# Kernel tuning notes

Hardware: AMD Instinct MI355X
Metric: run time of the kernel (lower is better)

Reference implementation:

```python
import jax, jax.numpy as jnp
import numpy as np

N_LOOPS, B, L, V = 4, 4, 256, 50257

def setup_inputs() -> dict:
    key = jax.random.key(0)
    k1, k2, k3, k4 = jax.random.split(key, 4)
    logits = jax.random.normal(k1, (N_LOOPS, B, L, V), dtype=jnp.float32)
    input_ids = jax.random.randint(k2, (B, L), 0, V)
    ans_starts = jax.random.randint(k3, (B,), 1, L)
    # draw chain targets from tokens that actually appear in input_ids so the
    # restricted-vocab validity check (tgt in unique(input_ids[b])) passes
    pos = jax.random.randint(k4, (B, N_LOOPS), 0, L)
    chain_targets = jnp.take_along_axis(input_ids, pos, axis=1)  # [B, N_LOOPS]
    return {"logits": logits, "input_ids": input_ids,
            "ans_starts": ans_starts, "chain_targets": chain_targets}

def reference(logits, input_ids, ans_starts, chain_targets):
    # logits:        [n_loops, B, L, V]  per-loop lm_head outputs
    # input_ids:     [B, L] int
    # ans_starts:    [B] int (answer position; logits read at as_-1)
    # chain_targets: [B, n_loops] int target token ids per loop
    n_loops, Bb, Ll, Vv = logits.shape
    # restricted-vocab mask: 0 where token appears in the prompt, -inf elsewhere
    # (replaces the per-sample torch.unique + scatter loop)
    valid_tok = jnp.zeros((Bb, Vv), dtype=bool).at[
        jnp.arange(Bb)[:, None], input_ids].set(True)          # [B, V]
    mask = jnp.where(valid_tok, 0.0, -jnp.inf)                  # [B, V]

    as_idx = jnp.clip(ans_starts - 1, 0, Ll - 1)                # [B]
    # gather logits at the answer position for every loop: [n_loops, B, V]
    la = logits[:, jnp.arange(Bb), as_idx, :]
    masked = la + mask[None]                                    # [n_loops, B, V]

    tgt = chain_targets.T                                       # [n_loops, B]
    pos_ok = (ans_starts >= 1) & (ans_starts < Ll)              # [B]
    tgt_ok = valid_tok[jnp.arange(Bb)[None, :], tgt]            # [n_loops, B]
    valid = pos_ok[None, :] & tgt_ok                            # [n_loops, B]

    pred = jnp.argmax(masked, axis=-1)                          # [n_loops, B]
    safe_tgt = jnp.where(valid, tgt, pred)  # keep CE finite for invalid rows
    logp = jax.nn.log_softmax(masked, axis=-1)
    ce = -jnp.take_along_axis(logp, safe_tgt[..., None], axis=-1)[..., 0]
    acc = (pred == tgt).astype(jnp.float32)

    vf = valid.astype(jnp.float32)
    cnt = vf.sum(axis=1)                                        # [n_loops]
    loop_loss = (ce * vf).sum(axis=1) / jnp.maximum(cnt, 1.0)
    loop_acc = (acc * vf).sum(axis=1) / jnp.maximum(cnt, 1.0)
    has = (cnt > 0).astype(jnp.float32)
    n_valid_loops = jnp.maximum(has.sum(), 1.0)
    avg_loss = (loop_loss * has).sum() / n_valid_loops
    avg_acc = (loop_acc * has).sum() / n_valid_loops
    final_loop_acc = loop_acc[-1]
    return avg_loss, avg_acc, final_loop_acc
```

## Files before the change

kernel.cpp:

```cpp
#include <hip/hip_runtime.h>
#include <hip/hip_bf16.h>
#include <math.h>


#define NL 4
#define BB 4
#define LL 256
#define VV 50257
#define VWORDS ((VV + 31) / 32)
#define TPB 1024

__global__ __launch_bounds__(TPB) void rowstat_kernel(
    const float* __restrict__ logits,
    const int* __restrict__ input_ids,
    const int* __restrict__ ans_starts,
    const int* __restrict__ chain_targets,
    float* __restrict__ ws)
{
    const int nb = blockIdx.x;
    const int n = nb / BB;
    const int b = nb % BB;
    const int tid = threadIdx.x;

    __shared__ unsigned bitmap[VWORDS];
    __shared__ float sm[TPB];
    __shared__ float ss[TPB];
    __shared__ int   si[TPB];

    for (int i = tid; i < VWORDS; i += TPB) bitmap[i] = 0u;
    __syncthreads();
    for (int i = tid; i < LL; i += TPB) {
        int t = input_ids[b * LL + i];
        atomicOr(&bitmap[t >> 5], 1u << (t & 31));
    }
    __syncthreads();

    const int as = ans_starts[b];
    const bool pos_ok = (as >= 1) && (as < LL);
    int as_idx = as - 1;
    if (as_idx < 0) as_idx = 0;
    if (as_idx > LL - 1) as_idx = LL - 1;

    const float* row = logits + (((size_t)n * BB + b) * LL + as_idx) * (size_t)VV;

    float m = -INFINITY;
    float s = 0.0f;
    int am = 0x7fffffff;
    for (int v = tid; v < VV; v += TPB) {
        if ((bitmap[v >> 5] >> (v & 31)) & 1u) {
            float x = row[v];
            if (x > m) {
                s = s * expf(m - x) + 1.0f;
                m = x;
                am = v;
            } else {
                s += expf(x - m);
            }
        }
    }

    sm[tid] = m; ss[tid] = s; si[tid] = am;
    __syncthreads();

    for (int off = TPB / 2; off > 0; off >>= 1) {
        if (tid < off) {
            float m1 = sm[tid],       s1 = ss[tid];       int i1 = si[tid];
            float m2 = sm[tid + off], s2 = ss[tid + off]; int i2 = si[tid + off];
            int ni = (m2 > m1 || (m2 == m1 && i2 < i1)) ? i2 : i1;
            float nm, ns;
            if (m1 == -INFINITY)      { nm = m2; ns = s2; }
            else if (m2 == -INFINITY) { nm = m1; ns = s1; }
            else {
                nm = fmaxf(m1, m2);
                ns = s1 * expf(m1 - nm) + s2 * expf(m2 - nm);
            }
            sm[tid] = nm; ss[tid] = ns; si[tid] = ni;
        }
        __syncthreads();
    }

    if (tid == 0) {
        const int tgt = chain_targets[b * NL + n];
        const bool tgt_ok = ((bitmap[tgt >> 5] >> (tgt & 31)) & 1u) != 0u;
        const bool valid = pos_ok && tgt_ok;
        const float maxv = sm[0];
        const float sumv = ss[0];
        const int pred = si[0];

        float ce = 0.0f, ac = 0.0f, vf = 0.0f;
        if (valid) {
            vf = 1.0f;
            float lt = row[tgt];
            ce = -(lt - maxv - logf(sumv));
            ac = (pred == tgt) ? 1.0f : 0.0f;
        }
        float* w = ws + (size_t)nb * 3;
        w[0] = ce; w[1] = ac; w[2] = vf;
    }
}

__global__ void finalize_kernel(const float* __restrict__ ws, float* __restrict__ out)
{
    if (blockIdx.x == 0 && threadIdx.x == 0) {
        float loss_num = 0.0f, acc_num = 0.0f, has_sum = 0.0f, final_acc = 0.0f;
        for (int n = 0; n < NL; ++n) {
            float ce = 0.0f, ac = 0.0f, cnt = 0.0f;
            for (int b = 0; b < BB; ++b) {
                const float* w = ws + (size_t)(n * BB + b) * 3;
                ce  += w[0];
                ac  += w[1];
                cnt += w[2];
            }
            float denom = fmaxf(cnt, 1.0f);
            float ll = ce / denom;
            float la = ac / denom;
            float has = (cnt > 0.0f) ? 1.0f : 0.0f;
            loss_num += ll * has;
            acc_num  += la * has;
            has_sum  += has;
            if (n == NL - 1) final_acc = la;
        }
        float nv = fmaxf(has_sum, 1.0f);
        out[0] = loss_num / nv;
        out[1] = acc_num / nv;
        out[2] = final_acc;
    }
}

extern "C" void kernel_launch(void* const* d_in, const int* in_sizes, int n_in,
                              void* d_out, int out_size, void* d_ws, size_t ws_size,
                              hipStream_t stream) {
    const float* logits        = (const float*)d_in[0];
    const int*   input_ids     = (const int*)d_in[1];
    const int*   ans_starts    = (const int*)d_in[2];
    const int*   chain_targets = (const int*)d_in[3];
    float* out = (float*)d_out;
    float* ws  = (float*)d_ws;

    rowstat_kernel<<<dim3(NL * BB), dim3(TPB), 0, stream>>>(
        logits, input_ids, ans_starts, chain_targets, ws);
    finalize_kernel<<<dim3(1), dim3(64), 0, stream>>>(ws, out);
}
```

Measured before the change: 867.5 us.

## Gather only unique prompt tokens instead of scanning the full vocabulary

```diff
diff --git a/kernel.cpp b/kernel.cpp
--- a/kernel.cpp
+++ b/kernel.cpp
@@ -8,7 +8,7 @@
 #define LL 256
 #define VV 50257
 #define VWORDS ((VV + 31) / 32)
-#define TPB 1024
+#define TPB 256
 
 __global__ __launch_bounds__(TPB) void rowstat_kernel(
     const float* __restrict__ logits,
@@ -23,17 +23,27 @@
     const int tid = threadIdx.x;
 
     __shared__ unsigned bitmap[VWORDS];
+    __shared__ int toks[LL];
+    __shared__ unsigned ucnt;
     __shared__ float sm[TPB];
     __shared__ float ss[TPB];
     __shared__ int   si[TPB];
 
     for (int i = tid; i < VWORDS; i += TPB) bitmap[i] = 0u;
+    if (tid == 0) ucnt = 0u;
     __syncthreads();
-    for (int i = tid; i < LL; i += TPB) {
-        int t = input_ids[b * LL + i];
-        atomicOr(&bitmap[t >> 5], 1u << (t & 31));
+
+    {
+        int t = input_ids[b * LL + tid];
+        unsigned bit = 1u << (t & 31);
+        unsigned old = atomicOr(&bitmap[t >> 5], bit);
+        if (!(old & bit)) {
+            unsigned p = atomicAdd(&ucnt, 1u);
+            toks[p] = t;
+        }
     }
     __syncthreads();
+    const int K = (int)ucnt;
 
     const int as = ans_starts[b];
     const bool pos_ok = (as >= 1) && (as < LL);
@@ -43,39 +53,31 @@
 
     const float* row = logits + (((size_t)n * BB + b) * LL + as_idx) * (size_t)VV;
 
-    float m = -INFINITY;
-    float s = 0.0f;
-    int am = 0x7fffffff;
-    for (int v = tid; v < VV; v += TPB) {
-        if ((bitmap[v >> 5] >> (v & 31)) & 1u) {
-            float x = row[v];
-            if (x > m) {
-                s = s * expf(m - x) + 1.0f;
-                m = x;
-                am = v;
-            } else {
-                s += expf(x - m);
-            }
-        }
+    float x = -INFINITY;
+    int   idx = 0x7fffffff;
+    if (tid < K) {
+        idx = toks[tid];
+        x = row[idx];
     }
 
-    sm[tid] = m; ss[tid] = s; si[tid] = am;
+    sm[tid] = x; si[tid] = idx;
+    __syncthreads();
+    for (int off = TPB / 2; off > 0; off >>= 1) {
+        if (tid < off) {
+            float m1 = sm[tid], m2 = sm[tid + off];
+            int   i1 = si[tid], i2 = si[tid + off];
+            if (m2 > m1 || (m2 == m1 && i2 < i1)) { sm[tid] = m2; si[tid] = i2; }
+        }
+        __syncthreads();
+    }
+    const float m = sm[0];
+    const int pred = si[0];
     __syncthreads();
 
+    ss[tid] = (tid < K) ? expf(x - m) : 0.0f;
+    __syncthreads();
     for (int off = TPB / 2; off > 0; off >>= 1) {
-        if (tid < off) {
-            float m1 = sm[tid],       s1 = ss[tid];       int i1 = si[tid];
-            float m2 = sm[tid + off], s2 = ss[tid + off]; int i2 = si[tid + off];
-            int ni = (m2 > m1 || (m2 == m1 && i2 < i1)) ? i2 : i1;
-            float nm, ns;
-            if (m1 == -INFINITY)      { nm = m2; ns = s2; }
-            else if (m2 == -INFINITY) { nm = m1; ns = s1; }
-            else {
-                nm = fmaxf(m1, m2);
-                ns = s1 * expf(m1 - nm) + s2 * expf(m2 - nm);
-            }
-            sm[tid] = nm; ss[tid] = ns; si[tid] = ni;
-        }
+        if (tid < off) ss[tid] += ss[tid + off];
         __syncthreads();
     }
 
@@ -83,15 +85,12 @@
         const int tgt = chain_targets[b * NL + n];
         const bool tgt_ok = ((bitmap[tgt >> 5] >> (tgt & 31)) & 1u) != 0u;
         const bool valid = pos_ok && tgt_ok;
-        const float maxv = sm[0];
-        const float sumv = ss[0];
-        const int pred = si[0];
 
         float ce = 0.0f, ac = 0.0f, vf = 0.0f;
         if (valid) {
             vf = 1.0f;
             float lt = row[tgt];
-            ce = -(lt - maxv - logf(sumv));
+            ce = -(lt - m - logf(ss[0]));
             ac = (pred == tgt) ? 1.0f : 0.0f;
         }
         float* w = ws + (size_t)nb * 3;
```

New measurement: 856.4 us. About the same (-1.3%).
